# Optimization experiments

Hardware: AMD Instinct MI355X
Metric: run time of the kernel (lower is better)

The kernel has to match this reference:

```python
import jax, jax.numpy as jnp
import numpy as np

B, T, H = 32, 2048, 1024


def setup_inputs() -> dict:
    key = jax.random.key(0)
    k1, k2, k3, k4, k5 = jax.random.split(key, 5)
    hidden = jax.random.normal(k1, (1, B, H), dtype=jnp.float32)
    encoder_outputs = jax.random.normal(k2, (B, T, H), dtype=jnp.float32)
    # nn.Linear(2H, H): weight [H, 2H], bias [H]
    lim = 1.0 / np.sqrt(2 * H)
    W = jax.random.uniform(k3, (H, 2 * H), minval=-lim, maxval=lim, dtype=jnp.float32)
    b = jax.random.uniform(k4, (H,), minval=-lim, maxval=lim, dtype=jnp.float32)
    stdv = 1.0 / np.sqrt(H)
    v = jax.random.uniform(k5, (H,), minval=-stdv, maxval=stdv, dtype=jnp.float32)
    return {"hidden": hidden, "encoder_outputs": encoder_outputs, "W": W, "b": b, "v": v}


def reference(hidden, encoder_outputs, W, b, v):
    # hidden: [1, B, H] -> broadcast to [B, T, H]
    h = jnp.broadcast_to(jnp.transpose(hidden, (1, 0, 2)), encoder_outputs.shape)
    x = jnp.concatenate([h, encoder_outputs], axis=2)          # [B, T, 2H]
    energy = jnp.tanh(jnp.einsum('btd,hd->bth', x, W) + b)      # [B, T, H]
    scores = jnp.einsum('h,bth->bt', v, energy)[:, None, :]     # [B, 1, T]
    return jax.nn.softmax(scores, axis=2)
```

## Files before the change

kernel.cpp:

```cpp
#include <hip/hip_runtime.h>
#include <hip/hip_bf16.h>

#define H 1024
#define T 2048
#define B 32
#define BK 128
#define NCHUNK 8

typedef __attribute__((ext_vector_type(8))) __bf16 bf16x8;
typedef __attribute__((ext_vector_type(16))) float f32x16;
typedef __attribute__((ext_vector_type(8))) unsigned short u16x8;

__device__ __forceinline__ unsigned short f2bf(float f) {
    unsigned int x = __float_as_uint(f);
    x += 0x7fffu + ((x >> 16) & 1u);
    return (unsigned short)(x >> 16);
}

__device__ __forceinline__ float fast_tanh(float x) {
    float t = __expf(2.0f * x);
    return 1.0f - 2.0f * __builtin_amdgcn_rcpf(t + 1.0f);
}

__global__ __launch_bounds__(256) void prep_w_kernel(const float* __restrict__ W,
                                                     unsigned short* __restrict__ Wp) {
    int gid = blockIdx.x * 256 + threadIdx.x;
    int n = gid & (H - 1);
    int kg = gid >> 10;
    const float* srcp = W + (size_t)n * (2 * H) + H + kg * 8;
    float4 f0 = *(const float4*)(srcp);
    float4 f1 = *(const float4*)(srcp + 4);
    u16x8 o;
    o[0] = f2bf(f0.x); o[1] = f2bf(f0.y); o[2] = f2bf(f0.z); o[3] = f2bf(f0.w);
    o[4] = f2bf(f1.x); o[5] = f2bf(f1.y); o[6] = f2bf(f1.z); o[7] = f2bf(f1.w);
    *(u16x8*)(Wp + (size_t)gid * 8) = o;
}

__global__ __launch_bounds__(128) void prep_hp_kernel(const float* __restrict__ hidden,
                                                      const float* __restrict__ W,
                                                      const float* __restrict__ bias,
                                                      float* __restrict__ hp) {
    int b = blockIdx.y;
    int h = blockIdx.x * 128 + threadIdx.x;
    const float* hid = hidden + (size_t)b * H;
    const float* wr = W + (size_t)h * (2 * H);
    float acc = 0.f;
    for (int d = 0; d < H; d += 4) {
        float4 wv = *(const float4*)(wr + d);
        float4 hv = *(const float4*)(hid + d);
        acc += wv.x * hv.x + wv.y * hv.y + wv.z * hv.z + wv.w * hv.w;
    }
    hp[(size_t)b * H + h] = acc + bias[h];
}

__global__ __launch_bounds__(512, 2) void energy_kernel(const float* __restrict__ enc,
                                                        const float* __restrict__ hp,
                                                        const float* __restrict__ vvec,
                                                        const unsigned short* __restrict__ Wp,
                                                        float* __restrict__ scores) {
    __shared__ __align__(16) unsigned short Abuf[2][NCHUNK * 1024];
    __shared__ float scpart[8][64];

    const int tid = threadIdx.x;
    const int b = blockIdx.y;
    const int t0 = blockIdx.x * 64;
    const int wave = tid >> 6;
    const int lane = tid & 63;
    const int l31 = lane & 31;
    const int hi = lane >> 5;

    const float* st_src = enc + ((size_t)b * T + t0 + lane) * H + wave * 16;
    char* st_dst = (char*)&Abuf[0][0] + wave * 2048 + lane * 16;

    const char* Abase = (const char*)&Abuf[0][0];
    const int a_off = hi * 1024 + l31 * 16;

    const unsigned short* wp_col = Wp + (size_t)(wave * 128 + l31) * 8 + (size_t)hi * (H * 8);

    f32x16 acc[2][4];
#pragma unroll
    for (int rg = 0; rg < 2; ++rg)
#pragma unroll
        for (int cg = 0; cg < 4; ++cg)
#pragma unroll
            for (int i = 0; i < 16; ++i) acc[rg][cg][i] = 0.f;

    {
        float4 f0 = *(const float4*)(st_src + 0);
        float4 f1 = *(const float4*)(st_src + 4);
        float4 f2 = *(const float4*)(st_src + 8);
        float4 f3 = *(const float4*)(st_src + 12);
        u16x8 o0, o1;
        o0[0] = f2bf(f0.x); o0[1] = f2bf(f0.y); o0[2] = f2bf(f0.z); o0[3] = f2bf(f0.w);
        o0[4] = f2bf(f1.x); o0[5] = f2bf(f1.y); o0[6] = f2bf(f1.z); o0[7] = f2bf(f1.w);
        o1[0] = f2bf(f2.x); o1[1] = f2bf(f2.y); o1[2] = f2bf(f2.z); o1[3] = f2bf(f2.w);
        o1[4] = f2bf(f3.x); o1[5] = f2bf(f3.y); o1[6] = f2bf(f3.z); o1[7] = f2bf(f3.w);
        *(u16x8*)(st_dst) = o0;
        *(u16x8*)(st_dst + 1024) = o1;
    }
    __syncthreads();

    for (int j = 0; j < NCHUNK; ++j) {
        float4 f0, f1, f2, f3;
        const bool pf = (j < NCHUNK - 1);
        if (pf) {
            const float* p = st_src + (j + 1) * BK;
            f0 = *(const float4*)(p + 0);
            f1 = *(const float4*)(p + 4);
            f2 = *(const float4*)(p + 8);
            f3 = *(const float4*)(p + 12);
        }
        const char* Ab = Abase + (j & 1) * 16384;
        const unsigned short* wpj = wp_col + (size_t)(j * 16) * (H * 8);
#pragma unroll
        for (int ki = 0; ki < 8; ++ki) {
            bf16x8 a0 = *(const bf16x8*)(Ab + ki * 2048 + a_off);
            bf16x8 a1 = *(const bf16x8*)(Ab + ki * 2048 + a_off + 512);
            const unsigned short* wpk = wpj + (size_t)(ki * 2) * (H * 8);
            bf16x8 b0 = *(const bf16x8*)(wpk + 0 * 256);
            bf16x8 b1 = *(const bf16x8*)(wpk + 1 * 256);
            bf16x8 b2 = *(const bf16x8*)(wpk + 2 * 256);
            bf16x8 b3 = *(const bf16x8*)(wpk + 3 * 256);
            acc[0][0] = __builtin_amdgcn_mfma_f32_32x32x16_bf16(a0, b0, acc[0][0], 0, 0, 0);
            acc[0][1] = __builtin_amdgcn_mfma_f32_32x32x16_bf16(a0, b1, acc[0][1], 0, 0, 0);
            acc[0][2] = __builtin_amdgcn_mfma_f32_32x32x16_bf16(a0, b2, acc[0][2], 0, 0, 0);
            acc[0][3] = __builtin_amdgcn_mfma_f32_32x32x16_bf16(a0, b3, acc[0][3], 0, 0, 0);
            acc[1][0] = __builtin_amdgcn_mfma_f32_32x32x16_bf16(a1, b0, acc[1][0], 0, 0, 0);
            acc[1][1] = __builtin_amdgcn_mfma_f32_32x32x16_bf16(a1, b1, acc[1][1], 0, 0, 0);
            acc[1][2] = __builtin_amdgcn_mfma_f32_32x32x16_bf16(a1, b2, acc[1][2], 0, 0, 0);
            acc[1][3] = __builtin_amdgcn_mfma_f32_32x32x16_bf16(a1, b3, acc[1][3], 0, 0, 0);
        }
        if (pf) {
            u16x8 o0, o1;
            o0[0] = f2bf(f0.x); o0[1] = f2bf(f0.y); o0[2] = f2bf(f0.z); o0[3] = f2bf(f0.w);
            o0[4] = f2bf(f1.x); o0[5] = f2bf(f1.y); o0[6] = f2bf(f1.z); o0[7] = f2bf(f1.w);
            o1[0] = f2bf(f2.x); o1[1] = f2bf(f2.y); o1[2] = f2bf(f2.z); o1[3] = f2bf(f2.w);
            o1[4] = f2bf(f3.x); o1[5] = f2bf(f3.y); o1[6] = f2bf(f3.z); o1[7] = f2bf(f3.w);
            char* dst = st_dst + ((j + 1) & 1) * 16384;
            *(u16x8*)dst = o0;
            *(u16x8*)(dst + 1024) = o1;
        }
        __syncthreads();
    }

    float pscore[2][16];
#pragma unroll
    for (int rg = 0; rg < 2; ++rg)
#pragma unroll
        for (int r = 0; r < 16; ++r) pscore[rg][r] = 0.f;

    const size_t bH = (size_t)b * H;
#pragma unroll
    for (int cg = 0; cg < 4; ++cg) {
        const int col = wave * 128 + cg * 32 + l31;
        const float hpv = hp[bH + col];
        const float vv = vvec[col];
#pragma unroll
        for (int rg = 0; rg < 2; ++rg)
#pragma unroll
            for (int r = 0; r < 16; ++r)
                pscore[rg][r] += vv * fast_tanh(acc[rg][cg][r] + hpv);
    }

#pragma unroll
    for (int rg = 0; rg < 2; ++rg)
#pragma unroll
        for (int r = 0; r < 16; ++r) {
            float s = pscore[rg][r];
            s += __shfl_xor(s, 1);
            s += __shfl_xor(s, 2);
            s += __shfl_xor(s, 4);
            s += __shfl_xor(s, 8);
            s += __shfl_xor(s, 16);
            pscore[rg][r] = s;
        }
    if (l31 == 0) {
#pragma unroll
        for (int rg = 0; rg < 2; ++rg)
#pragma unroll
            for (int r = 0; r < 16; ++r) {
                int m = (r & 3) + 8 * (r >> 2) + 4 * hi + rg * 32;
                scpart[wave][m] = pscore[rg][r];
            }
    }
    __syncthreads();
    if (tid < 64) {
        float s = 0.f;
#pragma unroll
        for (int w = 0; w < 8; ++w) s += scpart[w][tid];
        scores[(size_t)b * T + t0 + tid] = s;
    }
}

__global__ __launch_bounds__(256) void softmax_kernel(const float* __restrict__ sc,
                                                      float* __restrict__ out) {
    int b = blockIdx.x;
    int tid = threadIdx.x;
    int wave = tid >> 6, lane = tid & 63;
    const float* row = sc + (size_t)b * T;
    float vals[8];
    float m = -1e30f;
#pragma unroll
    for (int i = 0; i < 8; ++i) { vals[i] = row[tid + 256 * i]; m = fmaxf(m, vals[i]); }
#pragma unroll
    for (int s = 1; s < 64; s <<= 1) m = fmaxf(m, __shfl_xor(m, s));
    __shared__ float red[4];
    __shared__ float red2[4];
    if (lane == 0) red[wave] = m;
    __syncthreads();
    m = fmaxf(fmaxf(red[0], red[1]), fmaxf(red[2], red[3]));
    float sum = 0.f;
#pragma unroll
    for (int i = 0; i < 8; ++i) { vals[i] = expf(vals[i] - m); sum += vals[i]; }
#pragma unroll
    for (int s = 1; s < 64; s <<= 1) sum += __shfl_xor(sum, s);
    if (lane == 0) red2[wave] = sum;
    __syncthreads();
    sum = red2[0] + red2[1] + red2[2] + red2[3];
    float inv = 1.0f / sum;
#pragma unroll
    for (int i = 0; i < 8; ++i) out[(size_t)b * T + tid + 256 * i] = vals[i] * inv;
}

extern "C" void kernel_launch(void* const* d_in, const int* in_sizes, int n_in,
                              void* d_out, int out_size, void* d_ws, size_t ws_size,
                              hipStream_t stream) {
    (void)in_sizes; (void)n_in; (void)out_size; (void)ws_size;
    const float* hidden = (const float*)d_in[0];
    const float* enc    = (const float*)d_in[1];
    const float* W      = (const float*)d_in[2];
    const float* bias   = (const float*)d_in[3];
    const float* v      = (const float*)d_in[4];
    float* out = (float*)d_out;

    unsigned short* Wp = (unsigned short*)d_ws;
    float* hp = (float*)((char*)d_ws + 2 * 1024 * 1024);
    float* sc = (float*)((char*)d_ws + 2 * 1024 * 1024 + 128 * 1024);

    prep_w_kernel<<<dim3(512), dim3(256), 0, stream>>>(W, Wp);
    prep_hp_kernel<<<dim3(8, B), dim3(128), 0, stream>>>(hidden, W, bias, hp);
    energy_kernel<<<dim3(T / 64, B), dim3(512), 0, stream>>>(enc, hp, v, Wp, sc);
    softmax_kernel<<<dim3(B), dim3(256), 0, stream>>>(sc, out);
}
```

Baseline: 246.6 us.

## Split energy kernel work across 16 waves with XOR-swizzled LDS staging

Each energy block now has 1024 threads (16 waves), so each wave covers 64 output columns instead of 128. Accumulator registers per wave drop by half, which should allow more waves per CU and better latency hiding. Staging now gives each thread one 8-element k-slice, and LDS addresses are XOR-swizzled to avoid bank conflicts. The cost is more B-operand traffic from global memory relative to the MFMA work per wave, plus a larger cross-wave reduction.

```diff
diff --git a/kernel.cpp b/kernel.cpp
--- a/kernel.cpp
+++ b/kernel.cpp
@@ -53,13 +53,13 @@
     hp[(size_t)b * H + h] = acc + bias[h];
 }
 
-__global__ __launch_bounds__(512, 2) void energy_kernel(const float* __restrict__ enc,
-                                                        const float* __restrict__ hp,
-                                                        const float* __restrict__ vvec,
-                                                        const unsigned short* __restrict__ Wp,
-                                                        float* __restrict__ scores) {
+__global__ __launch_bounds__(1024, 4) void energy_kernel(const float* __restrict__ enc,
+                                                         const float* __restrict__ hp,
+                                                         const float* __restrict__ vvec,
+                                                         const unsigned short* __restrict__ Wp,
+                                                         float* __restrict__ scores) {
     __shared__ __align__(16) unsigned short Abuf[2][NCHUNK * 1024];
-    __shared__ float scpart[8][64];
+    __shared__ float scpart[16][64];
 
     const int tid = threadIdx.x;
     const int b = blockIdx.y;
@@ -69,76 +69,63 @@
     const int l31 = lane & 31;
     const int hi = lane >> 5;
 
-    const float* st_src = enc + ((size_t)b * T + t0 + lane) * H + wave * 16;
-    char* st_dst = (char*)&Abuf[0][0] + wave * 2048 + lane * 16;
+    const int st_row = tid >> 4;
+    const int st_ks = tid & 15;
+    const float* st_src = enc + ((size_t)b * T + t0 + st_row) * H + st_ks * 8;
+    char* st_dst = (char*)&Abuf[0][0] + st_ks * 1024 + ((st_row ^ (st_ks & 7)) * 16);
 
     const char* Abase = (const char*)&Abuf[0][0];
-    const int a_off = hi * 1024 + l31 * 16;
-
-    const unsigned short* wp_col = Wp + (size_t)(wave * 128 + l31) * 8 + (size_t)hi * (H * 8);
-
-    f32x16 acc[2][4];
+    const int l31x = l31;
+
+    const unsigned short* wp_col = Wp + (size_t)(wave * 64 + l31) * 8 + (size_t)hi * (H * 8);
+
+    f32x16 acc[2][2];
 #pragma unroll
     for (int rg = 0; rg < 2; ++rg)
 #pragma unroll
-        for (int cg = 0; cg < 4; ++cg)
+        for (int cg = 0; cg < 2; ++cg)
 #pragma unroll
             for (int i = 0; i < 16; ++i) acc[rg][cg][i] = 0.f;
 
     {
         float4 f0 = *(const float4*)(st_src + 0);
         float4 f1 = *(const float4*)(st_src + 4);
-        float4 f2 = *(const float4*)(st_src + 8);
-        float4 f3 = *(const float4*)(st_src + 12);
-        u16x8 o0, o1;
-        o0[0] = f2bf(f0.x); o0[1] = f2bf(f0.y); o0[2] = f2bf(f0.z); o0[3] = f2bf(f0.w);
-        o0[4] = f2bf(f1.x); o0[5] = f2bf(f1.y); o0[6] = f2bf(f1.z); o0[7] = f2bf(f1.w);
-        o1[0] = f2bf(f2.x); o1[1] = f2bf(f2.y); o1[2] = f2bf(f2.z); o1[3] = f2bf(f2.w);
-        o1[4] = f2bf(f3.x); o1[5] = f2bf(f3.y); o1[6] = f2bf(f3.z); o1[7] = f2bf(f3.w);
-        *(u16x8*)(st_dst) = o0;
-        *(u16x8*)(st_dst + 1024) = o1;
+        u16x8 o;
+        o[0] = f2bf(f0.x); o[1] = f2bf(f0.y); o[2] = f2bf(f0.z); o[3] = f2bf(f0.w);
+        o[4] = f2bf(f1.x); o[5] = f2bf(f1.y); o[6] = f2bf(f1.z); o[7] = f2bf(f1.w);
+        *(u16x8*)(st_dst) = o;
     }
     __syncthreads();
 
     for (int j = 0; j < NCHUNK; ++j) {
-        float4 f0, f1, f2, f3;
+        float4 f0, f1;
         const bool pf = (j < NCHUNK - 1);
         if (pf) {
             const float* p = st_src + (j + 1) * BK;
             f0 = *(const float4*)(p + 0);
             f1 = *(const float4*)(p + 4);
-            f2 = *(const float4*)(p + 8);
-            f3 = *(const float4*)(p + 12);
         }
         const char* Ab = Abase + (j & 1) * 16384;
         const unsigned short* wpj = wp_col + (size_t)(j * 16) * (H * 8);
 #pragma unroll
         for (int ki = 0; ki < 8; ++ki) {
-            bf16x8 a0 = *(const bf16x8*)(Ab + ki * 2048 + a_off);
-            bf16x8 a1 = *(const bf16x8*)(Ab + ki * 2048 + a_off + 512);
+            const int kslot = ki * 2 + hi;
+            const char* ap = Ab + kslot * 1024 + ((l31x ^ (kslot & 7)) * 16);
+            bf16x8 a0 = *(const bf16x8*)(ap);
+            bf16x8 a1 = *(const bf16x8*)(ap + 512);
             const unsigned short* wpk = wpj + (size_t)(ki * 2) * (H * 8);
             bf16x8 b0 = *(const bf16x8*)(wpk + 0 * 256);
             bf16x8 b1 = *(const bf16x8*)(wpk + 1 * 256);
-            bf16x8 b2 = *(const bf16x8*)(wpk + 2 * 256);
-            bf16x8 b3 = *(const bf16x8*)(wpk + 3 * 256);
             acc[0][0] = __builtin_amdgcn_mfma_f32_32x32x16_bf16(a0, b0, acc[0][0], 0, 0, 0);
             acc[0][1] = __builtin_amdgcn_mfma_f32_32x32x16_bf16(a0, b1, acc[0][1], 0, 0, 0);
-            acc[0][2] = __builtin_amdgcn_mfma_f32_32x32x16_bf16(a0, b2, acc[0][2], 0, 0, 0);
-            acc[0][3] = __builtin_amdgcn_mfma_f32_32x32x16_bf16(a0, b3, acc[0][3], 0, 0, 0);
             acc[1][0] = __builtin_amdgcn_mfma_f32_32x32x16_bf16(a1, b0, acc[1][0], 0, 0, 0);
             acc[1][1] = __builtin_amdgcn_mfma_f32_32x32x16_bf16(a1, b1, acc[1][1], 0, 0, 0);
-            acc[1][2] = __builtin_amdgcn_mfma_f32_32x32x16_bf16(a1, b2, acc[1][2], 0, 0, 0);
-            acc[1][3] = __builtin_amdgcn_mfma_f32_32x32x16_bf16(a1, b3, acc[1][3], 0, 0, 0);
         }
         if (pf) {
-            u16x8 o0, o1;
-            o0[0] = f2bf(f0.x); o0[1] = f2bf(f0.y); o0[2] = f2bf(f0.z); o0[3] = f2bf(f0.w);
-            o0[4] = f2bf(f1.x); o0[5] = f2bf(f1.y); o0[6] = f2bf(f1.z); o0[7] = f2bf(f1.w);
-            o1[0] = f2bf(f2.x); o1[1] = f2bf(f2.y); o1[2] = f2bf(f2.z); o1[3] = f2bf(f2.w);
-            o1[4] = f2bf(f3.x); o1[5] = f2bf(f3.y); o1[6] = f2bf(f3.z); o1[7] = f2bf(f3.w);
-            char* dst = st_dst + ((j + 1) & 1) * 16384;
-            *(u16x8*)dst = o0;
-            *(u16x8*)(dst + 1024) = o1;
+            u16x8 o;
+            o[0] = f2bf(f0.x); o[1] = f2bf(f0.y); o[2] = f2bf(f0.z); o[3] = f2bf(f0.w);
+            o[4] = f2bf(f1.x); o[5] = f2bf(f1.y); o[6] = f2bf(f1.z); o[7] = f2bf(f1.w);
+            *(u16x8*)(st_dst + ((j + 1) & 1) * 16384) = o;
         }
         __syncthreads();
     }
@@ -151,8 +138,8 @@
 
     const size_t bH = (size_t)b * H;
 #pragma unroll
-    for (int cg = 0; cg < 4; ++cg) {
-        const int col = wave * 128 + cg * 32 + l31;
+    for (int cg = 0; cg < 2; ++cg) {
+        const int col = wave * 64 + cg * 32 + l31;
         const float hpv = hp[bH + col];
         const float vv = vvec[col];
 #pragma unroll
@@ -187,7 +174,7 @@
     if (tid < 64) {
         float s = 0.f;
 #pragma unroll
-        for (int w = 0; w < 8; ++w) s += scpart[w][tid];
+        for (int w = 0; w < 16; ++w) s += scpart[w][tid];
         scores[(size_t)b * T + t0 + tid] = s;
     }
 }
@@ -239,6 +226,6 @@
 
     prep_w_kernel<<<dim3(512), dim3(256), 0, stream>>>(W, Wp);
     prep_hp_kernel<<<dim3(8, B), dim3(128), 0, stream>>>(hidden, W, bias, hp);
-    energy_kernel<<<dim3(T / 64, B), dim3(512), 0, stream>>>(enc, hp, v, Wp, sc);
+    energy_kernel<<<dim3(T / 64, B), dim3(1024), 0, stream>>>(enc, hp, v, Wp, sc);
     softmax_kernel<<<dim3(B), dim3(256), 0, stream>>>(sc, out);
 }
```

Result: no change. 244.2 us (-1.0%).

## Retile energy GEMM to 128-row blocks split over two column halves

Applied to the files above, without the earlier changes.

The energy kernel now processes 128 time rows per block and splits the H output columns into two 512-wide halves across a new grid dimension. Each wave computes a 4x2 grid of MFMA tiles instead of 2x4, so each W fragment is reused over more rows. The A tile in LDS uses an XOR swizzle to avoid bank conflicts, and B fragments are register double-buffered one k-step ahead. Partial scores for each column half are written separately and summed in the softmax kernel. The cost is the extra partial-score buffer plus more registers per thread, which may reduce occupancy.

```diff
diff --git a/kernel.cpp b/kernel.cpp
--- a/kernel.cpp
+++ b/kernel.cpp
@@ -4,8 +4,11 @@
 #define H 1024
 #define T 2048
 #define B 32
-#define BK 128
-#define NCHUNK 8
+#define BM 128
+#define BKC 64
+#define NCHUNK 16
+#define NCOLT 2
+#define BCOLS 512
 
 typedef __attribute__((ext_vector_type(8))) __bf16 bf16x8;
 typedef __attribute__((ext_vector_type(16))) float f32x16;
@@ -20,6 +23,10 @@
 __device__ __forceinline__ float fast_tanh(float x) {
     float t = __expf(2.0f * x);
     return 1.0f - 2.0f * __builtin_amdgcn_rcpf(t + 1.0f);
+}
+
+__device__ __forceinline__ int rswz(int r) {
+    return (r << 4) ^ ((r & 0x38) << 1);
 }
 
 __global__ __launch_bounds__(256) void prep_w_kernel(const float* __restrict__ W,
@@ -53,142 +60,167 @@
     hp[(size_t)b * H + h] = acc + bias[h];
 }
 
+#define MFMA32(A, Bv, C) __builtin_amdgcn_mfma_f32_32x32x16_bf16(A, Bv, C, 0, 0, 0)
+
 __global__ __launch_bounds__(512, 2) void energy_kernel(const float* __restrict__ enc,
                                                         const float* __restrict__ hp,
                                                         const float* __restrict__ vvec,
                                                         const unsigned short* __restrict__ Wp,
-                                                        float* __restrict__ scores) {
-    __shared__ __align__(16) unsigned short Abuf[2][NCHUNK * 1024];
-    __shared__ float scpart[8][64];
+                                                        float* __restrict__ sc_part) {
+    __shared__ __align__(16) unsigned short Abuf[2][BM * BKC];
+    __shared__ float scpart[8][BM];
 
     const int tid = threadIdx.x;
-    const int b = blockIdx.y;
-    const int t0 = blockIdx.x * 64;
+    const int b = blockIdx.z;
+    const int t0 = blockIdx.x * BM;
+    const int c0 = blockIdx.y * BCOLS;
     const int wave = tid >> 6;
     const int lane = tid & 63;
     const int l31 = lane & 31;
     const int hi = lane >> 5;
 
-    const float* st_src = enc + ((size_t)b * T + t0 + lane) * H + wave * 16;
-    char* st_dst = (char*)&Abuf[0][0] + wave * 2048 + lane * 16;
-
-    const char* Abase = (const char*)&Abuf[0][0];
-    const int a_off = hi * 1024 + l31 * 16;
-
-    const unsigned short* wp_col = Wp + (size_t)(wave * 128 + l31) * 8 + (size_t)hi * (H * 8);
-
-    f32x16 acc[2][4];
-#pragma unroll
-    for (int rg = 0; rg < 2; ++rg)
-#pragma unroll
-        for (int cg = 0; cg < 4; ++cg)
+    const int st_ks = tid & 7;
+    const int st_rb = tid >> 3;
+    const int r0 = st_rb * 2, r1 = r0 + 1;
+    const float* st_src0 = enc + ((size_t)b * T + t0 + r0) * H + st_ks * 8;
+    const float* st_src1 = st_src0 + H;
+    char* Ab0 = (char*)&Abuf[0][0];
+    char* st_d0 = Ab0 + st_ks * 2048 + rswz(r0);
+    char* st_d1 = Ab0 + st_ks * 2048 + rswz(r1);
+
+    const int a_off0 = rswz(0 * 32 + l31);
+    const int a_off1 = rswz(1 * 32 + l31);
+    const int a_off2 = rswz(2 * 32 + l31);
+    const int a_off3 = rswz(3 * 32 + l31);
+
+    const unsigned short* wp_base = Wp + (size_t)(c0 + wave * 64 + l31) * 8 + (size_t)hi * (H * 8);
+
+    f32x16 acc[4][2];
+#pragma unroll
+    for (int rg = 0; rg < 4; ++rg)
+#pragma unroll
+        for (int cg = 0; cg < 2; ++cg)
 #pragma unroll
             for (int i = 0; i < 16; ++i) acc[rg][cg][i] = 0.f;
 
     {
-        float4 f0 = *(const float4*)(st_src + 0);
-        float4 f1 = *(const float4*)(st_src + 4);
-        float4 f2 = *(const float4*)(st_src + 8);
-        float4 f3 = *(const float4*)(st_src + 12);
+        float4 f0 = *(const float4*)(st_src0);
+        float4 f1 = *(const float4*)(st_src0 + 4);
+        float4 f2 = *(const float4*)(st_src1);
+        float4 f3 = *(const float4*)(st_src1 + 4);
         u16x8 o0, o1;
         o0[0] = f2bf(f0.x); o0[1] = f2bf(f0.y); o0[2] = f2bf(f0.z); o0[3] = f2bf(f0.w);
         o0[4] = f2bf(f1.x); o0[5] = f2bf(f1.y); o0[6] = f2bf(f1.z); o0[7] = f2bf(f1.w);
         o1[0] = f2bf(f2.x); o1[1] = f2bf(f2.y); o1[2] = f2bf(f2.z); o1[3] = f2bf(f2.w);
         o1[4] = f2bf(f3.x); o1[5] = f2bf(f3.y); o1[6] = f2bf(f3.z); o1[7] = f2bf(f3.w);
-        *(u16x8*)(st_dst) = o0;
-        *(u16x8*)(st_dst + 1024) = o1;
-    }
-    __syncthreads();
+        *(u16x8*)st_d0 = o0;
+        *(u16x8*)st_d1 = o1;
+    }
+    bf16x8 bpe0 = *(const bf16x8*)(wp_base);
+    bf16x8 bpe1 = *(const bf16x8*)(wp_base + 256);
+    bf16x8 bpo0, bpo1;
+    __syncthreads();
+
+#define KI_STEP(KI, CUR0, CUR1, NXT0, NXT1)                                   \
+    {                                                                          \
+        const int it = j * 4 + (KI);                                           \
+        if (it < 63) {                                                         \
+            const unsigned short* bp = wp_base + (size_t)(it + 1) * (H * 16);  \
+            NXT0 = *(const bf16x8*)(bp);                                       \
+            NXT1 = *(const bf16x8*)(bp + 256);                                 \
+        }                                                                      \
+        const char* ap = Ab + (((KI) * 2 + hi) * 2048);                        \
+        bf16x8 a0 = *(const bf16x8*)(ap + a_off0);                             \
+        bf16x8 a1 = *(const bf16x8*)(ap + a_off1);                             \
+        bf16x8 a2 = *(const bf16x8*)(ap + a_off2);                             \
+        bf16x8 a3 = *(const bf16x8*)(ap + a_off3);                             \
+        acc[0][0] = MFMA32(a0, CUR0, acc[0][0]);                               \
+        acc[0][1] = MFMA32(a0, CUR1, acc[0][1]);                               \
+        acc[1][0] = MFMA32(a1, CUR0, acc[1][0]);                               \
+        acc[1][1] = MFMA32(a1, CUR1, acc[1][1]);                               \
+        acc[2][0] = MFMA32(a2, CUR0, acc[2][0]);                               \
+        acc[2][1] = MFMA32(a2, CUR1, acc[2][1]);                               \
+        acc[3][0] = MFMA32(a3, CUR0, acc[3][0]);                               \
+        acc[3][1] = MFMA32(a3, CUR1, acc[3][1]);                               \
+    }
 
     for (int j = 0; j < NCHUNK; ++j) {
         float4 f0, f1, f2, f3;
         const bool pf = (j < NCHUNK - 1);
         if (pf) {
-            const float* p = st_src + (j + 1) * BK;
-            f0 = *(const float4*)(p + 0);
-            f1 = *(const float4*)(p + 4);
-            f2 = *(const float4*)(p + 8);
-            f3 = *(const float4*)(p + 12);
+            const float* p0 = st_src0 + (j + 1) * BKC;
+            const float* p1 = st_src1 + (j + 1) * BKC;
+            f0 = *(const float4*)(p0);
+            f1 = *(const float4*)(p0 + 4);
+            f2 = *(const float4*)(p1);
+            f3 = *(const float4*)(p1 + 4);
         }
-        const char* Ab = Abase + (j & 1) * 16384;
-        const unsigned short* wpj = wp_col + (size_t)(j * 16) * (H * 8);
-#pragma unroll
-        for (int ki = 0; ki < 8; ++ki) {
-            bf16x8 a0 = *(const bf16x8*)(Ab + ki * 2048 + a_off);
-            bf16x8 a1 = *(const bf16x8*)(Ab + ki * 2048 + a_off + 512);
-            const unsigned short* wpk = wpj + (size_t)(ki * 2) * (H * 8);
-            bf16x8 b0 = *(const bf16x8*)(wpk + 0 * 256);
-            bf16x8 b1 = *(const bf16x8*)(wpk + 1 * 256);
-            bf16x8 b2 = *(const bf16x8*)(wpk + 2 * 256);
-            bf16x8 b3 = *(const bf16x8*)(wpk + 3 * 256);
-            acc[0][0] = __builtin_amdgcn_mfma_f32_32x32x16_bf16(a0, b0, acc[0][0], 0, 0, 0);
-            acc[0][1] = __builtin_amdgcn_mfma_f32_32x32x16_bf16(a0, b1, acc[0][1], 0, 0, 0);
-            acc[0][2] = __builtin_amdgcn_mfma_f32_32x32x16_bf16(a0, b2, acc[0][2], 0, 0, 0);
-            acc[0][3] = __builtin_amdgcn_mfma_f32_32x32x16_bf16(a0, b3, acc[0][3], 0, 0, 0);
-            acc[1][0] = __builtin_amdgcn_mfma_f32_32x32x16_bf16(a1, b0, acc[1][0], 0, 0, 0);
-            acc[1][1] = __builtin_amdgcn_mfma_f32_32x32x16_bf16(a1, b1, acc[1][1], 0, 0, 0);
-            acc[1][2] = __builtin_amdgcn_mfma_f32_32x32x16_bf16(a1, b2, acc[1][2], 0, 0, 0);
-            acc[1][3] = __builtin_amdgcn_mfma_f32_32x32x16_bf16(a1, b3, acc[1][3], 0, 0, 0);
-        }
+        const char* Ab = Ab0 + (j & 1) * 16384;
+        KI_STEP(0, bpe0, bpe1, bpo0, bpo1)
+        KI_STEP(1, bpo0, bpo1, bpe0, bpe1)
+        KI_STEP(2, bpe0, bpe1, bpo0, bpo1)
+        KI_STEP(3, bpo0, bpo1, bpe0, bpe1)
         if (pf) {
             u16x8 o0, o1;
             o0[0] = f2bf(f0.x); o0[1] = f2bf(f0.y); o0[2] = f2bf(f0.z); o0[3] = f2bf(f0.w);
             o0[4] = f2bf(f1.x); o0[5] = f2bf(f1.y); o0[6] = f2bf(f1.z); o0[7] = f2bf(f1.w);
             o1[0] = f2bf(f2.x); o1[1] = f2bf(f2.y); o1[2] = f2bf(f2.z); o1[3] = f2bf(f2.w);
             o1[4] = f2bf(f3.x); o1[5] = f2bf(f3.y); o1[6] = f2bf(f3.z); o1[7] = f2bf(f3.w);
-            char* dst = st_dst + ((j + 1) & 1) * 16384;
-            *(u16x8*)dst = o0;
-            *(u16x8*)(dst + 1024) = o1;
+            char* d0 = st_d0 + ((j + 1) & 1) * 16384;
+            char* d1 = st_d1 + ((j + 1) & 1) * 16384;
+            *(u16x8*)d0 = o0;
+            *(u16x8*)d1 = o1;
         }
         __syncthreads();
     }
-
-    float pscore[2][16];
-#pragma unroll
-    for (int rg = 0; rg < 2; ++rg)
-#pragma unroll
-        for (int r = 0; r < 16; ++r) pscore[rg][r] = 0.f;
+#undef KI_STEP
+
+    float psc[4][16];
+#pragma unroll
+    for (int rg = 0; rg < 4; ++rg)
+#pragma unroll
+        for (int r = 0; r < 16; ++r) psc[rg][r] = 0.f;
 
     const size_t bH = (size_t)b * H;
 #pragma unroll
-    for (int cg = 0; cg < 4; ++cg) {
-        const int col = wave * 128 + cg * 32 + l31;
+    for (int cg = 0; cg < 2; ++cg) {
+        const int col = c0 + wave * 64 + cg * 32 + l31;
         const float hpv = hp[bH + col];
         const float vv = vvec[col];
 #pragma unroll
-        for (int rg = 0; rg < 2; ++rg)
+        for (int rg = 0; rg < 4; ++rg)
 #pragma unroll
             for (int r = 0; r < 16; ++r)
-                pscore[rg][r] += vv * fast_tanh(acc[rg][cg][r] + hpv);
-    }
-
-#pragma unroll
-    for (int rg = 0; rg < 2; ++rg)
+                psc[rg][r] += vv * fast_tanh(acc[rg][cg][r] + hpv);
+    }
+
+#pragma unroll
+    for (int rg = 0; rg < 4; ++rg)
 #pragma unroll
         for (int r = 0; r < 16; ++r) {
-            float s = pscore[rg][r];
+            float s = psc[rg][r];
             s += __shfl_xor(s, 1);
             s += __shfl_xor(s, 2);
             s += __shfl_xor(s, 4);
             s += __shfl_xor(s, 8);
             s += __shfl_xor(s, 16);
-            pscore[rg][r] = s;
+            psc[rg][r] = s;
         }
     if (l31 == 0) {
 #pragma unroll
-        for (int rg = 0; rg < 2; ++rg)
+        for (int rg = 0; rg < 4; ++rg)
 #pragma unroll
             for (int r = 0; r < 16; ++r) {
-                int m = (r & 3) + 8 * (r >> 2) + 4 * hi + rg * 32;
-                scpart[wave][m] = pscore[rg][r];
+                int m = rg * 32 + (r & 3) + 8 * (r >> 2) + 4 * hi;
+                scpart[wave][m] = psc[rg][r];
             }
     }
     __syncthreads();
-    if (tid < 64) {
+    if (tid < BM) {
         float s = 0.f;
 #pragma unroll
         for (int w = 0; w < 8; ++w) s += scpart[w][tid];
-        scores[(size_t)b * T + t0 + tid] = s;
+        sc_part[((size_t)blockIdx.y * B + b) * T + t0 + tid] = s;
     }
 }
 
@@ -197,11 +229,16 @@
     int b = blockIdx.x;
     int tid = threadIdx.x;
     int wave = tid >> 6, lane = tid & 63;
-    const float* row = sc + (size_t)b * T;
+    const float* row0 = sc + (size_t)b * T;
+    const float* row1 = sc + ((size_t)B + b) * T;
     float vals[8];
     float m = -1e30f;
 #pragma unroll
-    for (int i = 0; i < 8; ++i) { vals[i] = row[tid + 256 * i]; m = fmaxf(m, vals[i]); }
+    for (int i = 0; i < 8; ++i) {
+        int idx = tid + 256 * i;
+        vals[i] = row0[idx] + row1[idx];
+        m = fmaxf(m, vals[i]);
+    }
 #pragma unroll
     for (int s = 1; s < 64; s <<= 1) m = fmaxf(m, __shfl_xor(m, s));
     __shared__ float red[4];
@@ -239,6 +276,6 @@
 
     prep_w_kernel<<<dim3(512), dim3(256), 0, stream>>>(W, Wp);
     prep_hp_kernel<<<dim3(8, B), dim3(128), 0, stream>>>(hidden, W, bias, hp);
-    energy_kernel<<<dim3(T / 64, B), dim3(512), 0, stream>>>(enc, hp, v, Wp, sc);
+    energy_kernel<<<dim3(T / BM, NCOLT, B), dim3(512), 0, stream>>>(enc, hp, v, Wp, sc);
     softmax_kernel<<<dim3(B), dim3(256), 0, stream>>>(sc, out);
 }
```

Result: faster. 235.9 us (-4.4%).
